# Performance work log

Measured on AMD Instinct MI355X. Metric: run time of the kernel, lower is better.

## Reference

```python
import jax, jax.numpy as jnp
import numpy as np

N, E, IN_DIM, HID, OUT = 50000, 600000, 128, 256, 128

def setup_inputs() -> dict:
    key = jax.random.key(0)
    k1, k2, k3, k4, k5, k6, k7 = jax.random.split(key, 7)
    h = jax.random.normal(k1, (N, IN_DIM), dtype=jnp.float32)
    src = jax.random.randint(k2, (E,), 0, N)
    dst = jax.random.randint(k3, (E,), 0, N)
    s1 = 1.0 / np.sqrt(2 * IN_DIM)
    s2 = 1.0 / np.sqrt(HID)
    W1 = jax.random.uniform(k4, (2 * IN_DIM, HID), minval=-s1, maxval=s1, dtype=jnp.float32)
    b1 = jax.random.uniform(k5, (HID,), minval=-s1, maxval=s1, dtype=jnp.float32)
    W2 = jax.random.uniform(k6, (HID, OUT), minval=-s2, maxval=s2, dtype=jnp.float32)
    b2 = jax.random.uniform(k7, (OUT,), minval=-s2, maxval=s2, dtype=jnp.float32)
    return {"h": h, "src": src, "dst": dst, "W1": W1, "b1": b1, "W2": W2, "b2": b2}

def reference(h, src, dst, W1, b1, W2, b2):
    n = h.shape[0]
    # copy_u + mean: gather src features, segment-sum at dst, divide by in-degree
    msg_sum = jax.ops.segment_sum(h[src], dst, num_segments=n)          # [N, D]
    deg = jax.ops.segment_sum(jnp.ones((src.shape[0],), h.dtype), dst, num_segments=n)
    h_neigh = msg_sum / jnp.maximum(deg, 1.0)[:, None]                  # zero-deg nodes -> 0
    h_total = jnp.concatenate([h, h_neigh], axis=1)                     # [N, 2D]
    out = (h_total @ W1 + b1) @ W2 + b2                                 # 2-layer MLP (no inner activation)
    return jax.nn.relu(out)
```

## Files before the change

### kernel.cpp

```cpp
#include <hip/hip_runtime.h>

#define N_NODES 50000
#define E_EDGES 600000
#define IN_DIM  128
#define HID     256
#define OUT_DIM 128
#define CAP     64
#define ZROW    N_NODES

#define RANGE_N 6250
#define CHUNK_E 2048
#define NB_FILL 2344
#define NB_HCVT 3125
#define NB_WCVT 384
#define NB_PREP (NB_FILL + NB_HCVT + NB_WCVT + 1)
#define NB_MLP  1563
#define BROWS   32

typedef __bf16 bf16x8 __attribute__((ext_vector_type(8)));
typedef float  f32x16 __attribute__((ext_vector_type(16)));
typedef unsigned short ushort8 __attribute__((ext_vector_type(8)));

__device__ __forceinline__ unsigned short f2bf(float f) {
    union { float f; unsigned int i; } v; v.f = f;
    unsigned int b = v.i;
    b += 0x7fffu + ((b >> 16) & 1u);
    return (unsigned short)(b >> 16);
}
__device__ __forceinline__ void acc2(unsigned u, float& a0, float& a1) {
    union { unsigned i; float f; } lo, hi;
    lo.i = u << 16; hi.i = u & 0xffff0000u;
    a0 += lo.f; a1 += hi.f;
}

__global__ void __launch_bounds__(256)
sage_prep(const int* __restrict__ src, const int* __restrict__ dst,
          int* __restrict__ counts, char* __restrict__ outb,
          const float* __restrict__ h, unsigned short* __restrict__ ht,
          const float* __restrict__ W1, const float* __restrict__ W2,
          unsigned short* __restrict__ w1sw, unsigned short* __restrict__ w2sw) {
    int b = blockIdx.x;
    if (b < NB_FILL) {
        int r = b & 7;
        int chunk = b >> 3;
        int e0 = chunk * CHUNK_E + threadIdx.x * 8;
        if (e0 < E_EDGES) {
            int lo = r * RANGE_N, hi = lo + RANGE_N;
            const int4 d0 = *(const int4*)(dst + e0);
            const int4 d1 = *(const int4*)(dst + e0 + 4);
            int dd[8] = {d0.x, d0.y, d0.z, d0.w, d1.x, d1.y, d1.z, d1.w};
            #pragma unroll
            for (int k = 0; k < 8; ++k) {
                int d = dd[k];
                if (d >= lo && d < hi) {
                    int s = src[e0 + k];
                    int sl = atomicAdd(counts + d, 1);
                    if (sl < CAP) *((int*)(outb + (size_t)d * 512 + 256) + sl) = s;
                }
            }
        }
    } else if (b < NB_FILL + NB_HCVT) {
        int idx = (b - NB_FILL) * 256 + threadIdx.x;
        int n = idx >> 4, g = idx & 15;
        const float4 v0 = *(const float4*)(h + (size_t)n * IN_DIM + g * 8);
        const float4 v1 = *(const float4*)(h + (size_t)n * IN_DIM + g * 8 + 4);
        ushort8 o;
        o[0] = f2bf(v0.x); o[1] = f2bf(v0.y); o[2] = f2bf(v0.z); o[3] = f2bf(v0.w);
        o[4] = f2bf(v1.x); o[5] = f2bf(v1.y); o[6] = f2bf(v1.z); o[7] = f2bf(v1.w);
        *(ushort8*)(ht + (size_t)n * 128 + g * 8) = o;
    } else if (b < NB_FILL + NB_HCVT + NB_WCVT) {
        int i1 = (b - NB_FILL - NB_HCVT) * 256 + threadIdx.x;
        if (i1 < 65536) {
            int j = i1 & 7, n = (i1 >> 3) & 255, g = (i1 >> 11) & 1, ks = (i1 >> 12) & 3, c = i1 >> 14;
            int k = c * 64 + ks * 16 + g * 8 + j;
            w1sw[i1] = f2bf(W1[(size_t)k * HID + n]);
        } else {
            int i2 = i1 - 65536;
            int j = i2 & 7, n = (i2 >> 3) & 127, g = (i2 >> 10) & 1, ks = (i2 >> 11) & 7, c = (i2 >> 14) & 1;
            int k = c * 128 + ks * 16 + g * 8 + j;
            w2sw[i2] = f2bf(W2[(size_t)k * OUT_DIM + n]);
        }
    } else {
        if (threadIdx.x < 64)
            *(unsigned*)(ht + (size_t)ZROW * 128 + threadIdx.x * 2) = 0u;
    }
}

__global__ void __launch_bounds__(256, 8)
sage_fused(const int* __restrict__ counts,
           const unsigned short* __restrict__ ht,
           const unsigned short* __restrict__ w1sw,
           const unsigned short* __restrict__ w2sw,
           const float* __restrict__ b1,
           const float* __restrict__ b2,
           float* out) {
    __shared__ unsigned short hid_s[BROWS][264];

    const int t = threadIdx.x;
    const int nw = t >> 6;
    const int lane = t & 63;
    const int lr = lane & 31;
    const int lg = lane >> 5;
    const int base = blockIdx.x * BROWS;

    {
        #pragma unroll 1
        for (int g = 0; g < 2; ++g) {
            const int m0 = nw * 8 + g * 4;
            float a0[4], a1[4];
            int deg[4], ent[4];
            const int* bk[4];
            int4 q[4];
            int em = 0;
            #pragma unroll
            for (int j = 0; j < 4; ++j) {
                a0[j] = 0.f; a1[j] = 0.f;
                int node = min(base + m0 + j, N_NODES - 1);
                deg[j] = __builtin_amdgcn_readfirstlane(counts[node]);
                ent[j] = min(deg[j], CAP);
                em = max(em, ent[j]);
                bk[j] = (const int*)((const char*)out + (size_t)node * 512 + 256);
                q[j] = *(const int4*)(bk[j]);
                unsigned self = *(const unsigned*)(ht + (size_t)node * 128 + lane * 2);
                *(unsigned*)(&hid_s[m0 + j][128 + lane * 2]) = self;
            }
            #pragma unroll 1
            for (int p = 0; p < em; p += 4) {
                int4 nx[4];
                #pragma unroll
                for (int j = 0; j < 4; ++j)
                    nx[j] = *(const int4*)(bk[j] + min(p + 4, CAP - 4));
                unsigned uu[16];
                #pragma unroll
                for (int k = 0; k < 4; ++k) {
                    #pragma unroll
                    for (int j = 0; j < 4; ++j) {
                        int idx = (k == 0) ? q[j].x : (k == 1) ? q[j].y
                                : (k == 2) ? q[j].z : q[j].w;
                        idx = __builtin_amdgcn_readfirstlane(idx);
                        idx = (p + k < ent[j]) ? idx : ZROW;
                        uu[k * 4 + j] = *(const unsigned*)(ht + (size_t)idx * 128 + lane * 2);
                    }
                }
                #pragma unroll
                for (int k = 0; k < 4; ++k) {
                    #pragma unroll
                    for (int j = 0; j < 4; ++j)
                        acc2(uu[k * 4 + j], a0[j], a1[j]);
                }
                #pragma unroll
                for (int j = 0; j < 4; ++j) q[j] = nx[j];
            }
            #pragma unroll
            for (int j = 0; j < 4; ++j) {
                float inv = 1.0f / (float)max(deg[j], 1);
                unsigned o = (unsigned)f2bf(a0[j] * inv) | ((unsigned)f2bf(a1[j] * inv) << 16);
                *(unsigned*)(&hid_s[m0 + j][lane * 2]) = o;
            }
        }
    }

    __syncthreads();

    f32x16 c1[2];
    #pragma unroll
    for (int e2 = 0; e2 < 16; ++e2) { c1[0][e2] = 0.f; c1[1][e2] = 0.f; }

    #pragma unroll
    for (int c = 0; c < 4; ++c) {
        bf16x8 a0[4];
        #pragma unroll
        for (int ks = 0; ks < 4; ++ks) {
            int koff = (c < 2) ? (128 + c * 64 + ks * 16 + lg * 8)
                               : ((c - 2) * 64 + ks * 16 + lg * 8);
            a0[ks] = *(const bf16x8*)(&hid_s[lr][koff]);
        }
        #pragma unroll
        for (int ks = 0; ks < 4; ++ks) {
            #pragma unroll
            for (int nt = 0; nt < 2; ++nt) {
                int n = nw * 64 + nt * 32 + lr;
                bf16x8 b = *(const bf16x8*)(w1sw + c * 16384 + (((ks * 2 + lg) * 256) + n) * 8);
                c1[nt] = __builtin_amdgcn_mfma_f32_32x32x16_bf16(a0[ks], b, c1[nt], 0, 0, 0);
            }
        }
    }

    __syncthreads();

    #pragma unroll
    for (int nt = 0; nt < 2; ++nt) {
        int col = nw * 64 + nt * 32 + lr;
        float bias = b1[col];
        #pragma unroll
        for (int reg = 0; reg < 16; ++reg) {
            int m = (reg & 3) + 8 * (reg >> 2) + 4 * lg;
            hid_s[m][col] = f2bf(c1[nt][reg] + bias);
        }
    }
    __syncthreads();

    f32x16 c2;
    #pragma unroll
    for (int e2 = 0; e2 < 16; ++e2) c2[e2] = 0.f;

    #pragma unroll
    for (int c = 0; c < 2; ++c) {
        #pragma unroll
        for (int ks = 0; ks < 8; ++ks) {
            bf16x8 b = *(const bf16x8*)(w2sw + c * 16384 + ((ks * 2 + lg) * 128 + nw * 32 + lr) * 8);
            int koff = c * 128 + ks * 16 + lg * 8;
            bf16x8 ah0 = *(const bf16x8*)(&hid_s[lr][koff]);
            c2 = __builtin_amdgcn_mfma_f32_32x32x16_bf16(ah0, b, c2, 0, 0, 0);
        }
    }

    {
        int col = nw * 32 + lr;
        float bias = b2[col];
        #pragma unroll
        for (int reg = 0; reg < 16; ++reg) {
            int m = (reg & 3) + 8 * (reg >> 2) + 4 * lg;
            int n = base + m;
            if (n < N_NODES)
                out[(size_t)n * OUT_DIM + col] = fmaxf(c2[reg] + bias, 0.0f);
        }
    }
}

extern "C" void kernel_launch(void* const* d_in, const int* in_sizes, int n_in,
                              void* d_out, int out_size, void* d_ws, size_t ws_size,
                              hipStream_t stream) {
    const float* h   = (const float*)d_in[0];
    const int*   src = (const int*)d_in[1];
    const int*   dst = (const int*)d_in[2];
    const float* W1  = (const float*)d_in[3];
    const float* b1  = (const float*)d_in[4];
    const float* W2  = (const float*)d_in[5];
    const float* b2  = (const float*)d_in[6];
    float* out = (float*)d_out;

    int* counts = (int*)d_ws;
    unsigned short* w1sw = (unsigned short*)(counts + N_NODES);
    unsigned short* w2sw = w1sw + 65536;
    unsigned short* ht   = w2sw + 32768;

    hipMemsetAsync(counts, 0, N_NODES * sizeof(int), stream);

    sage_prep<<<NB_PREP, 256, 0, stream>>>(
        src, dst, counts, (char*)d_out, h, ht, W1, W2, w1sw, w2sw);

    sage_fused<<<NB_MLP, 256, 0, stream>>>(counts, ht, w1sw, w2sw, b1, b2, out);
}
```

Baseline: 165.2 us.

## Replace global-atomic adjacency fill with LDS histogram, prefix scan, and fill passes

The per-edge global atomicAdd on node counts is replaced by a three-stage build: per-(chunk,range) shared-memory histograms stored as bytes, a per-node exclusive scan across chunks that yields counts and offsets, and a fill pass that uses LDS atomics to place source indices. This removes contended global atomics and the counts memset, at the cost of two extra kernel launches and a second read of dst. A fallback keeps the old path when the workspace is too small. Byte-sized histograms and offsets saturate at 255, and only 32 chunks are used, so each block scans a large edge range serially.

```diff
diff --git a/kernel.cpp b/kernel.cpp
--- a/kernel.cpp
+++ b/kernel.cpp
@@ -9,13 +9,19 @@
 #define ZROW    N_NODES
 
 #define RANGE_N 6250
-#define CHUNK_E 2048
-#define NB_FILL 2344
+#define NCHUNK  32
+#define CHUNK_E (E_EDGES / NCHUNK)
+#define NB_HIST 256
 #define NB_HCVT 3125
 #define NB_WCVT 384
-#define NB_PREP (NB_FILL + NB_HCVT + NB_WCVT + 1)
+#define NB_PREP (NB_HIST + NB_HCVT + NB_WCVT + 1)
+#define NB_CSR  196
 #define NB_MLP  1563
 #define BROWS   32
+
+#define FB_CHUNK_E 2048
+#define FB_NB_FILL 2344
+#define FB_NB_PREP (FB_NB_FILL + NB_HCVT + NB_WCVT + 1)
 
 typedef __bf16 bf16x8 __attribute__((ext_vector_type(8)));
 typedef float  f32x16 __attribute__((ext_vector_type(16)));
@@ -33,17 +39,118 @@
     a0 += lo.f; a1 += hi.f;
 }
 
+__device__ __forceinline__ void do_hcvt(int b0, int b, const float* __restrict__ h,
+                                        unsigned short* __restrict__ ht) {
+    int idx = (b - b0) * 256 + threadIdx.x;
+    int n = idx >> 4, g = idx & 15;
+    const float4 v0 = *(const float4*)(h + (size_t)n * IN_DIM + g * 8);
+    const float4 v1 = *(const float4*)(h + (size_t)n * IN_DIM + g * 8 + 4);
+    ushort8 o;
+    o[0] = f2bf(v0.x); o[1] = f2bf(v0.y); o[2] = f2bf(v0.z); o[3] = f2bf(v0.w);
+    o[4] = f2bf(v1.x); o[5] = f2bf(v1.y); o[6] = f2bf(v1.z); o[7] = f2bf(v1.w);
+    *(ushort8*)(ht + (size_t)n * 128 + g * 8) = o;
+}
+__device__ __forceinline__ void do_wcvt(int b0, int b,
+                                        const float* __restrict__ W1,
+                                        const float* __restrict__ W2,
+                                        unsigned short* __restrict__ w1sw,
+                                        unsigned short* __restrict__ w2sw) {
+    int i1 = (b - b0) * 256 + threadIdx.x;
+    if (i1 < 65536) {
+        int j = i1 & 7, n = (i1 >> 3) & 255, g = (i1 >> 11) & 1, ks = (i1 >> 12) & 3, c = i1 >> 14;
+        int k = c * 64 + ks * 16 + g * 8 + j;
+        w1sw[i1] = f2bf(W1[(size_t)k * HID + n]);
+    } else {
+        int i2 = i1 - 65536;
+        int j = i2 & 7, n = (i2 >> 3) & 127, g = (i2 >> 10) & 1, ks = (i2 >> 11) & 7, c = (i2 >> 14) & 1;
+        int k = c * 128 + ks * 16 + g * 8 + j;
+        w2sw[i2] = f2bf(W2[(size_t)k * OUT_DIM + n]);
+    }
+}
+
 __global__ void __launch_bounds__(256)
-sage_prep(const int* __restrict__ src, const int* __restrict__ dst,
-          int* __restrict__ counts, char* __restrict__ outb,
+sage_prep(const int* __restrict__ dst,
+          unsigned char* __restrict__ hist8,
           const float* __restrict__ h, unsigned short* __restrict__ ht,
           const float* __restrict__ W1, const float* __restrict__ W2,
           unsigned short* __restrict__ w1sw, unsigned short* __restrict__ w2sw) {
+    __shared__ unsigned lhist[RANGE_N];
     int b = blockIdx.x;
-    if (b < NB_FILL) {
+    if (b < NB_HIST) {
+        int r = b & 7, c = b >> 3;
+        for (int i = threadIdx.x; i < RANGE_N; i += 256) lhist[i] = 0u;
+        __syncthreads();
+        int lo = r * RANGE_N;
+        int e0 = c * CHUNK_E, e1 = e0 + CHUNK_E;
+        for (int e = e0 + threadIdx.x; e < e1; e += 256) {
+            int d = dst[e] - lo;
+            if ((unsigned)d < (unsigned)RANGE_N)
+                atomicAdd(&lhist[d], 1u);
+        }
+        __syncthreads();
+        unsigned char* hb = hist8 + (size_t)b * RANGE_N;
+        for (int i = threadIdx.x; i < RANGE_N; i += 256)
+            hb[i] = (unsigned char)min(lhist[i], 255u);
+    } else if (b < NB_HIST + NB_HCVT) {
+        do_hcvt(NB_HIST, b, h, ht);
+    } else if (b < NB_HIST + NB_HCVT + NB_WCVT) {
+        do_wcvt(NB_HIST + NB_HCVT, b, W1, W2, w1sw, w2sw);
+    } else {
+        if (threadIdx.x < 64)
+            *(unsigned*)(ht + (size_t)ZROW * 128 + threadIdx.x * 2) = 0u;
+    }
+}
+
+__global__ void __launch_bounds__(256)
+sage_csr(unsigned char* __restrict__ hist8, int* __restrict__ counts) {
+    int n = blockIdx.x * 256 + threadIdx.x;
+    if (n >= N_NODES) return;
+    int r = n / RANGE_N, nl = n - r * RANGE_N;
+    unsigned acc = 0;
+    #pragma unroll
+    for (int c = 0; c < NCHUNK; ++c) {
+        size_t idx = (size_t)(c * 8 + r) * RANGE_N + nl;
+        unsigned v = hist8[idx];
+        hist8[idx] = (unsigned char)acc;
+        acc += v;
+    }
+    counts[n] = (int)acc;
+}
+
+__global__ void __launch_bounds__(256)
+sage_fill(const int* __restrict__ src, const int* __restrict__ dst,
+          const unsigned char* __restrict__ hist8, char* __restrict__ outb) {
+    __shared__ unsigned lcur[RANGE_N];
+    int b = blockIdx.x;
+    int r = b & 7, c = b >> 3;
+    for (int i = threadIdx.x; i < RANGE_N; i += 256) lcur[i] = 0u;
+    __syncthreads();
+    int lo = r * RANGE_N;
+    int e0 = c * CHUNK_E, e1 = e0 + CHUNK_E;
+    const unsigned char* hb = hist8 + (size_t)b * RANGE_N;
+    for (int e = e0 + threadIdx.x; e < e1; e += 256) {
+        int d = dst[e];
+        int dl = d - lo;
+        if ((unsigned)dl < (unsigned)RANGE_N) {
+            int s = src[e];
+            unsigned slot = (unsigned)hb[dl] + atomicAdd(&lcur[dl], 1u);
+            if (slot < CAP)
+                *((int*)(outb + (size_t)d * 512 + 256) + slot) = s;
+        }
+    }
+}
+
+__global__ void __launch_bounds__(256)
+sage_prep_fb(const int* __restrict__ src, const int* __restrict__ dst,
+             int* __restrict__ counts, char* __restrict__ outb,
+             const float* __restrict__ h, unsigned short* __restrict__ ht,
+             const float* __restrict__ W1, const float* __restrict__ W2,
+             unsigned short* __restrict__ w1sw, unsigned short* __restrict__ w2sw) {
+    int b = blockIdx.x;
+    if (b < FB_NB_FILL) {
         int r = b & 7;
         int chunk = b >> 3;
-        int e0 = chunk * CHUNK_E + threadIdx.x * 8;
+        int e0 = chunk * FB_CHUNK_E + threadIdx.x * 8;
         if (e0 < E_EDGES) {
             int lo = r * RANGE_N, hi = lo + RANGE_N;
             const int4 d0 = *(const int4*)(dst + e0);
@@ -59,27 +166,10 @@
                 }
             }
         }
-    } else if (b < NB_FILL + NB_HCVT) {
-        int idx = (b - NB_FILL) * 256 + threadIdx.x;
-        int n = idx >> 4, g = idx & 15;
-        const float4 v0 = *(const float4*)(h + (size_t)n * IN_DIM + g * 8);
-        const float4 v1 = *(const float4*)(h + (size_t)n * IN_DIM + g * 8 + 4);
-        ushort8 o;
-        o[0] = f2bf(v0.x); o[1] = f2bf(v0.y); o[2] = f2bf(v0.z); o[3] = f2bf(v0.w);
-        o[4] = f2bf(v1.x); o[5] = f2bf(v1.y); o[6] = f2bf(v1.z); o[7] = f2bf(v1.w);
-        *(ushort8*)(ht + (size_t)n * 128 + g * 8) = o;
-    } else if (b < NB_FILL + NB_HCVT + NB_WCVT) {
-        int i1 = (b - NB_FILL - NB_HCVT) * 256 + threadIdx.x;
-        if (i1 < 65536) {
-            int j = i1 & 7, n = (i1 >> 3) & 255, g = (i1 >> 11) & 1, ks = (i1 >> 12) & 3, c = i1 >> 14;
-            int k = c * 64 + ks * 16 + g * 8 + j;
-            w1sw[i1] = f2bf(W1[(size_t)k * HID + n]);
-        } else {
-            int i2 = i1 - 65536;
-            int j = i2 & 7, n = (i2 >> 3) & 127, g = (i2 >> 10) & 1, ks = (i2 >> 11) & 7, c = (i2 >> 14) & 1;
-            int k = c * 128 + ks * 16 + g * 8 + j;
-            w2sw[i2] = f2bf(W2[(size_t)k * OUT_DIM + n]);
-        }
+    } else if (b < FB_NB_FILL + NB_HCVT) {
+        do_hcvt(FB_NB_FILL, b, h, ht);
+    } else if (b < FB_NB_FILL + NB_HCVT + NB_WCVT) {
+        do_wcvt(FB_NB_FILL + NB_HCVT, b, W1, W2, w1sw, w2sw);
     } else {
         if (threadIdx.x < 64)
             *(unsigned*)(ht + (size_t)ZROW * 128 + threadIdx.x * 2) = 0u;
@@ -241,14 +331,22 @@
     float* out = (float*)d_out;
 
     int* counts = (int*)d_ws;
-    unsigned short* w1sw = (unsigned short*)(counts + N_NODES);
-    unsigned short* w2sw = w1sw + 65536;
-    unsigned short* ht   = w2sw + 32768;
-
-    hipMemsetAsync(counts, 0, N_NODES * sizeof(int), stream);
-
-    sage_prep<<<NB_PREP, 256, 0, stream>>>(
-        src, dst, counts, (char*)d_out, h, ht, W1, W2, w1sw, w2sw);
+    unsigned short* w1sw = (unsigned short*)((char*)d_ws + 200000);
+    unsigned short* w2sw = (unsigned short*)((char*)d_ws + 331072);
+    unsigned short* ht   = (unsigned short*)((char*)d_ws + 396608);
+    unsigned char*  hist8 = (unsigned char*)((char*)d_ws + 13196864);
+    const size_t WS_CSR = 13196864 + (size_t)NB_HIST * RANGE_N;
+
+    if (ws_size >= WS_CSR) {
+        sage_prep<<<NB_PREP, 256, 0, stream>>>(
+            dst, hist8, h, ht, W1, W2, w1sw, w2sw);
+        sage_csr<<<NB_CSR, 256, 0, stream>>>(hist8, counts);
+        sage_fill<<<NB_HIST, 256, 0, stream>>>(src, dst, hist8, (char*)d_out);
+    } else {
+        hipMemsetAsync(counts, 0, N_NODES * sizeof(int), stream);
+        sage_prep_fb<<<FB_NB_PREP, 256, 0, stream>>>(
+            src, dst, counts, (char*)d_out, h, ht, W1, W2, w1sw, w2sw);
+    }
 
     sage_fused<<<NB_MLP, 256, 0, stream>>>(counts, ht, w1sw, w2sw, b1, b2, out);
 }
```

Result: slower. 212.7 us (+28.7%).
